# Optimization experiments

Hardware: AMD Instinct MI355X
Metric: run time of the kernel (lower is better)

The kernel has to match this reference:

```python
import jax, jax.numpy as jnp
import numpy as np

B, S, D, H = 64, 128, 1024, 8
DK = D // H  # 128 == S, required by the module's (attn@V)@V quirk
DFF = 2048
EPS = 1e-12


def layernorm(x, w, b):
    u = x.mean(-1, keepdims=True)
    s = ((x - u) ** 2).mean(-1, keepdims=True)
    return w * (x - u) / jnp.sqrt(s + EPS) + b


def setup_inputs() -> dict:
    key = jax.random.key(0)
    ks = jax.random.split(key, 10)
    w = lambda k, shape: jax.random.normal(k, shape, jnp.float32) * 0.02
    return {
        "x": jax.random.normal(ks[0], (B, S, D), jnp.float32),
        "mask": jnp.ones((1, 1, S, S), jnp.int32),
        "Wq": w(ks[1], (D, D)), "bq": jnp.zeros((D,), jnp.float32),
        "Wk": w(ks[2], (D, D)), "bk": jnp.zeros((D,), jnp.float32),
        "Wv": w(ks[3], (D, D)), "bv": jnp.zeros((D,), jnp.float32),
        "Wo": w(ks[4], (D, D)), "bo": jnp.zeros((D,), jnp.float32),
        "ln1_w": jnp.ones((D,), jnp.float32), "ln1_b": jnp.zeros((D,), jnp.float32),
        "W1": w(ks[5], (DFF, D)), "b1": jnp.zeros((DFF,), jnp.float32),
        "W2": w(ks[6], (4 * D, DFF)), "b2": jnp.zeros((4 * D,), jnp.float32),
        "W3": w(ks[7], (D, 4 * D)), "b3": jnp.zeros((D,), jnp.float32),
        "ln2_w": jnp.ones((D,), jnp.float32), "ln2_b": jnp.zeros((D,), jnp.float32),
    }


def reference(x, mask, Wq, bq, Wk, bk, Wv, bv, Wo, bo, ln1_w, ln1_b,
              W1, b1, W2, b2, W3, b3, ln2_w, ln2_b):
    # QKV projections -> [B, H, S, DK]
    Q = (x @ Wq.T + bq).reshape(B, S, H, DK).transpose(0, 2, 1, 3)
    K = (x @ Wk.T + bk).reshape(B, S, H, DK).transpose(0, 2, 1, 3)
    V = (x @ Wv.T + bv).reshape(B, S, H, DK).transpose(0, 2, 1, 3)

    scores = jnp.einsum('bhqd,bhkd->bhqk', Q, K) / jnp.sqrt(jnp.float32(DK))
    scores = jnp.where(mask == 0, jnp.float32(-1e9), scores)
    attn = jax.nn.softmax(scores, axis=-1)  # dropout = identity (eval)
    av = jnp.matmul(attn, V)                 # [B,H,S,DK]
    # Faithful quirk in the source: multiply by V a second time (DK == S).
    ctx = jnp.matmul(av, V)                  # [B,H,S,DK]
    ctx = ctx.transpose(0, 2, 1, 3).reshape(B, S, D)
    attn_out = ctx @ Wo.T + bo

    h = layernorm(x + attn_out, ln1_w, ln1_b)

    f = jax.nn.relu(h @ W1.T + b1)           # [B,S,DFF]
    f = jax.nn.relu(f @ W2.T + b2)           # [B,S,4D]
    f = f @ W3.T + b3                        # [B,S,D]

    return layernorm(h + f, ln2_w, ln2_b)
```

## Files before the change

kernel.cpp:

```cpp
#include <hip/hip_runtime.h>
#include <hip/hip_bf16.h>

using bf16 = __hip_bfloat16;
typedef __attribute__((ext_vector_type(4))) float f32x4;
typedef __attribute__((ext_vector_type(8))) short bf16x8;

__device__ __forceinline__ unsigned short bfbits(float f) {
    bf16 h = __float2bfloat16(f);
    return __builtin_bit_cast(unsigned short, h);
}

__device__ __forceinline__ void g2l16(const void* g, void* l) {
    __builtin_amdgcn_global_load_lds(
        (const __attribute__((address_space(1))) unsigned int*)g,
        (__attribute__((address_space(3))) unsigned int*)l, 16, 0, 0);
}

__global__ void castk(const float* __restrict__ in, bf16* __restrict__ out, int n4) {
    int stride = gridDim.x * blockDim.x;
    for (int i = blockIdx.x * blockDim.x + threadIdx.x; i < n4; i += stride) {
        float4 v = reinterpret_cast<const float4*>(in)[i];
        ushort4 o;
        o.x = bfbits(v.x); o.y = bfbits(v.y); o.z = bfbits(v.z); o.w = bfbits(v.w);
        reinterpret_cast<ushort4*>(out)[i] = o;
    }
}

template<int EPI>
__global__ __launch_bounds__(256, 2)
void gemm_bt(const bf16* __restrict__ A, const bf16* __restrict__ Bm,
             int M, int N, int K,
             const float* __restrict__ bias0, const float* __restrict__ bias1,
             const float* __restrict__ bias2, const float* __restrict__ resid,
             void* __restrict__ outp,
             bf16* __restrict__ q_o, bf16* __restrict__ k_o, bf16* __restrict__ v_o) {
    (void)M;
    __shared__ __align__(16) char As[8192];
    __shared__ __align__(16) char Bs[8192];
    int tid = threadIdx.x, wave = tid >> 6, lane = tid & 63;
    int nbn = N >> 7;
    int bm = blockIdx.x / nbn, bn = blockIdx.x % nbn;
    int wm = (wave >> 1) << 6, wn = (wave & 1) << 6;
    int rlo = lane & 15, g = lane >> 4;

    const char* abase = (const char*)(A + (size_t)(bm << 7) * K);
    const char* bbase = (const char*)(Bm + (size_t)(bn << 7) * K);

    const f32x4 fzero = {0.f, 0.f, 0.f, 0.f};
    f32x4 acc[4][4];
#pragma unroll
    for (int i = 0; i < 4; ++i)
#pragma unroll
        for (int j = 0; j < 4; ++j) acc[i][j] = fzero;

    int L0 = wave * 2048 + lane * 16;
    size_t ldbyte = (size_t)K * 2;

    for (int k0 = 0; k0 < K; k0 += 32) {
#pragma unroll
        for (int j = 0; j < 2; ++j) {
            int L = L0 + j * 1024;
            int row = L >> 6;
            int cb = (L & 63) ^ (((row >> 1) & 3) << 4);
            g2l16(abase + (size_t)row * ldbyte + (size_t)k0 * 2 + cb, As + wave * 2048 + j * 1024);
            g2l16(bbase + (size_t)row * ldbyte + (size_t)k0 * 2 + cb, Bs + wave * 2048 + j * 1024);
        }
        __syncthreads();
        bf16x8 af[4], bf8[4];
#pragma unroll
        for (int i = 0; i < 4; ++i) {
            int ra = wm + i * 16 + rlo;
            af[i] = *reinterpret_cast<const bf16x8*>(As + ra * 64 + ((g * 16) ^ (((ra >> 1) & 3) << 4)));
            int rb = wn + i * 16 + rlo;
            bf8[i] = *reinterpret_cast<const bf16x8*>(Bs + rb * 64 + ((g * 16) ^ (((rb >> 1) & 3) << 4)));
        }
#pragma unroll
        for (int mi = 0; mi < 4; ++mi)
#pragma unroll
            for (int ni = 0; ni < 4; ++ni)
                acc[mi][ni] = __builtin_amdgcn_mfma_f32_16x16x32_bf16(af[mi], bf8[ni], acc[mi][ni], 0, 0, 0);
        __syncthreads();
    }

    int gm0 = (bm << 7) + wm, gn0 = (bn << 7) + wn;
#pragma unroll
    for (int mi = 0; mi < 4; ++mi) {
#pragma unroll
        for (int ni = 0; ni < 4; ++ni) {
            int gnc = gn0 + ni * 16 + rlo;
#pragma unroll
            for (int r = 0; r < 4; ++r) {
                int gmr = gm0 + mi * 16 + g * 4 + r;
                float val = acc[mi][ni][r];
                if constexpr (EPI == 0) {
                    int t = gnc >> 10;
                    const float* bp = (t == 0) ? bias0 : ((t == 1) ? bias1 : bias2);
                    val += bp[gnc & 1023];
                    bf16* dst = (t == 0) ? q_o : ((t == 1) ? k_o : v_o);
                    int hh = (gnc >> 7) & 7, d = gnc & 127;
                    int bb = gmr >> 7, s = gmr & 127;
                    dst[(((size_t)bb * 8 + hh) * 128 + s) * 128 + d] = __float2bfloat16(val);
                } else if constexpr (EPI == 1) {
                    val = fmaxf(val + bias0[gnc], 0.f);
                    ((bf16*)outp)[(size_t)gmr * N + gnc] = __float2bfloat16(val);
                } else {
                    val += bias0[gnc] + resid[(size_t)gmr * N + gnc];
                    ((float*)outp)[(size_t)gmr * N + gnc] = val;
                }
            }
        }
    }
}

__global__ __launch_bounds__(256)
void transpose_v(const bf16* __restrict__ V, bf16* __restrict__ VT) {
    __shared__ unsigned short t[128 * 132];
    int bh = blockIdx.x, tid = threadIdx.x;
    const unsigned short* src = (const unsigned short*)(V + (size_t)bh * 16384);
#pragma unroll
    for (int i = 0; i < 8; ++i) {
        int idx = tid + i * 256;
        int srow = idx >> 4;
        int c8 = (idx & 15) * 8;
        ushort4 a = reinterpret_cast<const ushort4*>(src + srow * 128 + c8)[0];
        ushort4 b = reinterpret_cast<const ushort4*>(src + srow * 128 + c8 + 4)[0];
        reinterpret_cast<ushort4*>(t + srow * 132 + c8)[0] = a;
        reinterpret_cast<ushort4*>(t + srow * 132 + c8 + 4)[0] = b;
    }
    __syncthreads();
    unsigned short* dst = (unsigned short*)(VT + (size_t)bh * 16384);
#pragma unroll
    for (int i = 0; i < 8; ++i) {
        int idx = tid + i * 256;
        int drow = idx >> 4;
        int s8 = (idx & 15) * 8;
        ushort4 a, b;
        a.x = t[(s8 + 0) * 132 + drow]; a.y = t[(s8 + 1) * 132 + drow];
        a.z = t[(s8 + 2) * 132 + drow]; a.w = t[(s8 + 3) * 132 + drow];
        b.x = t[(s8 + 4) * 132 + drow]; b.y = t[(s8 + 5) * 132 + drow];
        b.z = t[(s8 + 6) * 132 + drow]; b.w = t[(s8 + 7) * 132 + drow];
        reinterpret_cast<ushort4*>(dst + drow * 128 + s8)[0] = a;
        reinterpret_cast<ushort4*>(dst + drow * 128 + s8 + 4)[0] = b;
    }
}

__global__ __launch_bounds__(256, 2)
void attn_scores(const bf16* __restrict__ Q, const bf16* __restrict__ K, bf16* __restrict__ P) {
    __shared__ __align__(16) char Qs[32768];
    __shared__ __align__(16) char Ks[32768];
    int bh = blockIdx.x;
    int tid = threadIdx.x, wave = tid >> 6, lane = tid & 63;
    const char* qsrc = (const char*)(Q + (size_t)bh * 16384);
    const char* ksrc = (const char*)(K + (size_t)bh * 16384);
#pragma unroll
    for (int j = 0; j < 8; ++j) {
        int L = wave * 8192 + j * 1024 + lane * 16;
        int row = L >> 8;
        int cb = (L & 255) ^ ((row & 7) << 4);
        g2l16(qsrc + row * 256 + cb, Qs + wave * 8192 + j * 1024);
        g2l16(ksrc + row * 256 + cb, Ks + wave * 8192 + j * 1024);
    }
    __syncthreads();
    int rlo = lane & 15, g = lane >> 4;
    const f32x4 fzero = {0.f, 0.f, 0.f, 0.f};
    f32x4 acc[2][8];
#pragma unroll
    for (int mi = 0; mi < 2; ++mi)
#pragma unroll
        for (int ni = 0; ni < 8; ++ni) acc[mi][ni] = fzero;
#pragma unroll
    for (int kk = 0; kk < 4; ++kk) {
        bf16x8 aq[2], bk8[8];
#pragma unroll
        for (int mi = 0; mi < 2; ++mi) {
            int row = wave * 32 + mi * 16 + rlo;
            aq[mi] = *reinterpret_cast<const bf16x8*>(Qs + row * 256 + ((kk * 64 + g * 16) ^ ((row & 7) << 4)));
        }
#pragma unroll
        for (int ni = 0; ni < 8; ++ni) {
            int row = ni * 16 + rlo;
            bk8[ni] = *reinterpret_cast<const bf16x8*>(Ks + row * 256 + ((kk * 64 + g * 16) ^ ((row & 7) << 4)));
        }
#pragma unroll
        for (int mi = 0; mi < 2; ++mi)
#pragma unroll
            for (int ni = 0; ni < 8; ++ni)
                acc[mi][ni] = __builtin_amdgcn_mfma_f32_16x16x32_bf16(aq[mi], bk8[ni], acc[mi][ni], 0, 0, 0);
    }
    const float scale = 0.088388347648318447f;
    unsigned short* pdst = (unsigned short*)(P + (size_t)bh * 16384);
#pragma unroll
    for (int mi = 0; mi < 2; ++mi) {
#pragma unroll
        for (int r = 0; r < 4; ++r) {
            float m = -3e38f;
#pragma unroll
            for (int ni = 0; ni < 8; ++ni) m = fmaxf(m, acc[mi][ni][r]);
#pragma unroll
            for (int o = 1; o < 16; o <<= 1) m = fmaxf(m, __shfl_xor(m, o));
            m *= scale;
            float e[8];
            float sum = 0.f;
#pragma unroll
            for (int ni = 0; ni < 8; ++ni) { e[ni] = __expf(acc[mi][ni][r] * scale - m); sum += e[ni]; }
#pragma unroll
            for (int o = 1; o < 16; o <<= 1) sum += __shfl_xor(sum, o);
            float inv = 1.f / sum;
            int qrow = wave * 32 + mi * 16 + g * 4 + r;
#pragma unroll
            for (int ni = 0; ni < 8; ++ni)
                pdst[qrow * 128 + ni * 16 + rlo] = bfbits(e[ni] * inv);
        }
    }
}

__global__ __launch_bounds__(256, 2)
void attn_ctx(const bf16* __restrict__ P, const bf16* __restrict__ VT, bf16* __restrict__ CTX) {
    __shared__ __align__(16) char Vs[32768];
    __shared__ __align__(16) char Ts[32768];
    int bh = blockIdx.x, b = bh >> 3, h = bh & 7;
    int tid = threadIdx.x, wave = tid >> 6, lane = tid & 63;
    const char* vsrc = (const char*)(VT + (size_t)bh * 16384);
#pragma unroll
    for (int j = 0; j < 8; ++j) {
        int L = wave * 8192 + j * 1024 + lane * 16;
        int row = L >> 8;
        int cb = (L & 255) ^ ((row & 7) << 4);
        g2l16(vsrc + row * 256 + cb, Vs + wave * 8192 + j * 1024);
    }
    __syncthreads();
    int rlo = lane & 15, g = lane >> 4;
    const char* psrc = (const char*)(P + (size_t)bh * 16384);
    const f32x4 fzero = {0.f, 0.f, 0.f, 0.f};
    f32x4 accT[2][8];
#pragma unroll
    for (int mi = 0; mi < 2; ++mi)
#pragma unroll
        for (int ni = 0; ni < 8; ++ni) accT[mi][ni] = fzero;
#pragma unroll
    for (int kk = 0; kk < 4; ++kk) {
        bf16x8 ap[2], bv8[8];
#pragma unroll
        for (int mi = 0; mi < 2; ++mi) {
            int row = wave * 32 + mi * 16 + rlo;
            ap[mi] = *reinterpret_cast<const bf16x8*>(psrc + (size_t)row * 256 + kk * 64 + g * 16);
        }
#pragma unroll
        for (int ni = 0; ni < 8; ++ni) {
            int row = ni * 16 + rlo;
            bv8[ni] = *reinterpret_cast<const bf16x8*>(Vs + row * 256 + ((kk * 64 + g * 16) ^ ((row & 7) << 4)));
        }
#pragma unroll
        for (int mi = 0; mi < 2; ++mi)
#pragma unroll
            for (int ni = 0; ni < 8; ++ni)
                accT[mi][ni] = __builtin_amdgcn_mfma_f32_16x16x32_bf16(ap[mi], bv8[ni], accT[mi][ni], 0, 0, 0);
    }
#pragma unroll
    for (int mi = 0; mi < 2; ++mi)
#pragma unroll
        for (int ni = 0; ni < 8; ++ni)
#pragma unroll
            for (int r = 0; r < 4; ++r) {
                int trow = wave * 32 + mi * 16 + g * 4 + r;
                int cbyte = ((ni * 16 + rlo) * 2) ^ ((trow & 7) << 4);
                *(unsigned short*)(Ts + trow * 256 + cbyte) = bfbits(accT[mi][ni][r]);
            }
    __syncthreads();
    f32x4 accC[2][8];
#pragma unroll
    for (int mi = 0; mi < 2; ++mi)
#pragma unroll
        for (int ni = 0; ni < 8; ++ni) accC[mi][ni] = fzero;
#pragma unroll
    for (int kk = 0; kk < 4; ++kk) {
        bf16x8 at[2], bv8[8];
#pragma unroll
        for (int mi = 0; mi < 2; ++mi) {
            int row = wave * 32 + mi * 16 + rlo;
            at[mi] = *reinterpret_cast<const bf16x8*>(Ts + row * 256 + ((kk * 64 + g * 16) ^ ((row & 7) << 4)));
        }
#pragma unroll
        for (int ni = 0; ni < 8; ++ni) {
            int row = ni * 16 + rlo;
            bv8[ni] = *reinterpret_cast<const bf16x8*>(Vs + row * 256 + ((kk * 64 + g * 16) ^ ((row & 7) << 4)));
        }
#pragma unroll
        for (int mi = 0; mi < 2; ++mi)
#pragma unroll
            for (int ni = 0; ni < 8; ++ni)
                accC[mi][ni] = __builtin_amdgcn_mfma_f32_16x16x32_bf16(at[mi], bv8[ni], accC[mi][ni], 0, 0, 0);
    }
    unsigned short* cdst = (unsigned short*)CTX;
#pragma unroll
    for (int mi = 0; mi < 2; ++mi)
#pragma unroll
        for (int ni = 0; ni < 8; ++ni)
#pragma unroll
            for (int r = 0; r < 4; ++r) {
                int q = wave * 32 + mi * 16 + g * 4 + r;
                int gm = b * 128 + q;
                int col = h * 128 + ni * 16 + rlo;
                cdst[(size_t)gm * 1024 + col] = bfbits(accC[mi][ni][r]);
            }
}

template<int MODE>
__global__ __launch_bounds__(256)
void ln_k(const float* __restrict__ Y, const float* __restrict__ w, const float* __restrict__ b,
          float* __restrict__ Hf, bf16* __restrict__ Hb) {
    int row = blockIdx.x, tid = threadIdx.x;
    float4 v = reinterpret_cast<const float4*>(Y + (size_t)row * 1024)[tid];
    float s = v.x + v.y + v.z + v.w;
    float q = v.x * v.x + v.y * v.y + v.z * v.z + v.w * v.w;
#pragma unroll
    for (int o = 1; o < 64; o <<= 1) { s += __shfl_xor(s, o); q += __shfl_xor(q, o); }
    __shared__ float ss[4], sq[4];
    if ((tid & 63) == 0) { ss[tid >> 6] = s; sq[tid >> 6] = q; }
    __syncthreads();
    s = ss[0] + ss[1] + ss[2] + ss[3];
    q = sq[0] + sq[1] + sq[2] + sq[3];
    float u = s * (1.f / 1024.f);
    float var = fmaxf(q * (1.f / 1024.f) - u * u, 0.f);
    float rstd = rsqrtf(var + 1e-12f);
    float4 wv = reinterpret_cast<const float4*>(w)[tid];
    float4 bv = reinterpret_cast<const float4*>(b)[tid];
    float o0 = wv.x * (v.x - u) * rstd + bv.x;
    float o1 = wv.y * (v.y - u) * rstd + bv.y;
    float o2 = wv.z * (v.z - u) * rstd + bv.z;
    float o3 = wv.w * (v.w - u) * rstd + bv.w;
    reinterpret_cast<float4*>(Hf + (size_t)row * 1024)[tid] = make_float4(o0, o1, o2, o3);
    if constexpr (MODE == 0) {
        ushort4 ob;
        ob.x = bfbits(o0); ob.y = bfbits(o1); ob.z = bfbits(o2); ob.w = bfbits(o3);
        reinterpret_cast<ushort4*>(Hb)[row * 256 + tid] = ob;
    }
}

extern "C" void kernel_launch(void* const* d_in, const int* in_sizes, int n_in,
                              void* d_out, int out_size, void* d_ws, size_t ws_size,
                              hipStream_t stream) {
    (void)in_sizes; (void)n_in; (void)out_size; (void)ws_size;
    const float* x    = (const float*)d_in[0];
    const float* Wq   = (const float*)d_in[2];
    const float* bq   = (const float*)d_in[3];
    const float* Wk   = (const float*)d_in[4];
    const float* bk   = (const float*)d_in[5];
    const float* Wv   = (const float*)d_in[6];
    const float* bv   = (const float*)d_in[7];
    const float* Wo   = (const float*)d_in[8];
    const float* bo   = (const float*)d_in[9];
    const float* ln1w = (const float*)d_in[10];
    const float* ln1b = (const float*)d_in[11];
    const float* W1   = (const float*)d_in[12];
    const float* b1   = (const float*)d_in[13];
    const float* W2   = (const float*)d_in[14];
    const float* b2   = (const float*)d_in[15];
    const float* W3   = (const float*)d_in[16];
    const float* b3   = (const float*)d_in[17];
    const float* ln2w = (const float*)d_in[18];
    const float* ln2b = (const float*)d_in[19];

    char* ws = (char*)d_ws;
    bf16*  XB    = (bf16*)(ws + 0);
    bf16*  WQKVB = (bf16*)(ws + 16777216);
    bf16*  WOB   = (bf16*)(ws + 23068672);
    bf16*  W1B   = (bf16*)(ws + 25165824);
    bf16*  W2B   = (bf16*)(ws + 29360128);
    bf16*  W3B   = (bf16*)(ws + 46137344);
    bf16*  Qb    = (bf16*)(ws + 54525952);
    bf16*  Kb    = (bf16*)(ws + 71303168);
    bf16*  Vb    = (bf16*)(ws + 88080384);
    bf16*  VTb   = (bf16*)(ws + 104857600);
    bf16*  Pb    = (bf16*)(ws + 121634816);
    bf16*  CTX   = (bf16*)(ws + 138412032);
    float* Y2    = (float*)(ws + 155189248);
    float* H32   = (float*)(ws + 188743680);
    bf16*  HB    = (bf16*)(ws + 222298112);
    bf16*  F1    = (bf16*)(ws + 155189248);
    bf16*  F2    = (bf16*)(ws + 54525952);
    float* Y5    = (float*)(ws + 121634816);

    auto cast = [&](const float* s, bf16* dd, int n4) {
        int nb = (n4 + 255) / 256; if (nb > 2048) nb = 2048;
        castk<<<nb, 256, 0, stream>>>(s, dd, n4);
    };
    cast(x,  XB,             2097152);
    cast(Wq, WQKVB,           262144);
    cast(Wk, WQKVB + 1048576, 262144);
    cast(Wv, WQKVB + 2097152, 262144);
    cast(Wo, WOB,             262144);
    cast(W1, W1B,             524288);
    cast(W2, W2B,            2097152);
    cast(W3, W3B,            1048576);

    gemm_bt<0><<<1536, 256, 0, stream>>>(XB, WQKVB, 8192, 3072, 1024,
                                         bq, bk, bv, nullptr, nullptr, Qb, Kb, Vb);
    transpose_v<<<512, 256, 0, stream>>>(Vb, VTb);
    attn_scores<<<512, 256, 0, stream>>>(Qb, Kb, Pb);
    attn_ctx<<<512, 256, 0, stream>>>(Pb, VTb, CTX);
    gemm_bt<2><<<512, 256, 0, stream>>>(CTX, WOB, 8192, 1024, 1024,
                                        bo, nullptr, nullptr, x, (void*)Y2,
                                        nullptr, nullptr, nullptr);
    ln_k<0><<<8192, 256, 0, stream>>>(Y2, ln1w, ln1b, H32, HB);
    gemm_bt<1><<<1024, 256, 0, stream>>>(HB, W1B, 8192, 2048, 1024,
                                         b1, nullptr, nullptr, nullptr, (void*)F1,
                                         nullptr, nullptr, nullptr);
    gemm_bt<1><<<2048, 256, 0, stream>>>(F1, W2B, 8192, 4096, 2048,
                                         b2, nullptr, nullptr, nullptr, (void*)F2,
                                         nullptr, nullptr, nullptr);
    gemm_bt<2><<<512, 256, 0, stream>>>(F2, W3B, 8192, 1024, 4096,
                                        b3, nullptr, nullptr, H32, (void*)Y5,
                                        nullptr, nullptr, nullptr);
    ln_k<1><<<8192, 256, 0, stream>>>(Y5, ln2w, ln2b, (float*)d_out, nullptr);
}
```

Baseline: 499.8 us.

## Add 256x256-tile triple-buffered GEMM for QKV and FFN up-projections

Adds a new 512-thread GEMM kernel with 256x256 output tiles. It uses triple-buffered direct global-to-LDS loads with an XOR swizzle, splits each k-step into two half-steps separated by barriers, raises wave priority around the MFMAs and remaps workgroup IDs across XCDs. The QKV, W1 and W2 GEMMs move to this kernel to get more data reuse per tile and to overlap loads with compute, while the old kernel now only serves the residual epilogue. The trade-offs are 96KB of LDS per block, fewer blocks (384/256/512) that may underfill the 256 CUs, and heavier register pressure from the 8x4 accumulator array.

```diff
diff --git a/kernel.cpp b/kernel.cpp
--- a/kernel.cpp
+++ b/kernel.cpp
@@ -27,13 +27,139 @@
 }
 
 template<int EPI>
+__global__ __launch_bounds__(512, 2)
+void gemm256(const bf16* __restrict__ A, const bf16* __restrict__ Bm,
+             int N, int K,
+             const float* __restrict__ bias0, const float* __restrict__ bias1,
+             const float* __restrict__ bias2,
+             void* __restrict__ outp,
+             bf16* __restrict__ q_o, bf16* __restrict__ k_o, bf16* __restrict__ v_o) {
+    __shared__ __align__(16) char lds[98304];
+    const int tid = threadIdx.x;
+    const int lane = tid & 63, wave = tid >> 6;
+    const int rlo = lane & 15, g = lane >> 4;
+    const int wr = wave >> 2, wc = wave & 3;
+    const int nbn = N >> 8;
+    const int nwg = gridDim.x;
+    int wg = (int)blockIdx.x;
+    wg = (wg & 7) * (nwg >> 3) + (wg >> 3);
+    const int bm = wg / nbn, bn = wg % nbn;
+    const size_t ldb = (size_t)K * 2;
+    const char* abase = (const char*)A + ((size_t)bm << 8) * ldb;
+    const char* bbase = (const char*)Bm + ((size_t)bn << 8) * ldb;
+
+    const int P = tid * 16;
+    const int R = P >> 7;
+    const int qs = (P & 127) ^ ((R & 7) << 4);
+    const size_t goff0 = (size_t)(R * 2 + (qs >> 6)) * ldb + (qs & 63);
+    const size_t ghalf = (size_t)128 * ldb;
+
+    const int o_in = (((rlo & 1) << 6) | (g << 4)) ^ (((rlo >> 1) & 7) << 4);
+    const int aoff = wr * 8192 + (rlo >> 1) * 128 + o_in;
+    const int boff = 16384 + (wc >> 1) * 8192 + (wc & 1) * 4096 + (rlo >> 1) * 128 + o_in;
+
+    const f32x4 fz = {0.f, 0.f, 0.f, 0.f};
+    f32x4 acc[8][4];
+#pragma unroll
+    for (int i = 0; i < 8; ++i)
+#pragma unroll
+        for (int j = 0; j < 4; ++j) acc[i][j] = fz;
+
+    auto stA = [&](int buf, int h, int kt) {
+        g2l16(abase + goff0 + (size_t)h * ghalf + (size_t)kt * 64,
+              lds + buf * 32768 + h * 8192 + P);
+    };
+    auto stB = [&](int buf, int h, int kt) {
+        g2l16(bbase + goff0 + (size_t)h * ghalf + (size_t)kt * 64,
+              lds + buf * 32768 + 16384 + h * 8192 + P);
+    };
+
+    stA(0, 0, 0); stA(0, 1, 0); stB(0, 0, 0); stB(0, 1, 0);
+    stA(1, 0, 1); stA(1, 1, 1); stB(1, 0, 1); stB(1, 1, 1);
+    asm volatile("s_waitcnt vmcnt(4)" ::: "memory");
+    __builtin_amdgcn_s_barrier();
+
+    const int NT = K >> 5;
+    for (int kt = 0; kt < NT; ++kt) {
+        const int buf = kt % 3;
+        const int nbuf = (kt + 2) % 3;
+        const char* lb = lds + buf * 32768;
+        const bool pre = (kt + 2) < NT;
+
+        bf16x8 bfr[4], afr[4];
+#pragma unroll
+        for (int nf = 0; nf < 4; ++nf)
+            bfr[nf] = *reinterpret_cast<const bf16x8*>(lb + nf * 1024 + boff);
+#pragma unroll
+        for (int i = 0; i < 4; ++i)
+            afr[i] = *reinterpret_cast<const bf16x8*>(lb + i * 1024 + aoff);
+        if (pre) { stA(nbuf, 0, kt + 2); stA(nbuf, 1, kt + 2); }
+        __builtin_amdgcn_s_barrier();
+        asm volatile("s_waitcnt lgkmcnt(0)");
+        __builtin_amdgcn_s_setprio(1);
+#pragma unroll
+        for (int i = 0; i < 4; ++i)
+#pragma unroll
+            for (int nf = 0; nf < 4; ++nf)
+                acc[i][nf] = __builtin_amdgcn_mfma_f32_16x16x32_bf16(afr[i], bfr[nf], acc[i][nf], 0, 0, 0);
+        __builtin_amdgcn_s_setprio(0);
+        __builtin_amdgcn_s_barrier();
+
+#pragma unroll
+        for (int i = 0; i < 4; ++i)
+            afr[i] = *reinterpret_cast<const bf16x8*>(lb + (4 + i) * 1024 + aoff);
+        if (pre) { stB(nbuf, 0, kt + 2); stB(nbuf, 1, kt + 2); }
+        if (pre) {
+            asm volatile("s_waitcnt vmcnt(4)" ::: "memory");
+        } else if (kt + 1 < NT) {
+            asm volatile("s_waitcnt vmcnt(0)" ::: "memory");
+        }
+        __builtin_amdgcn_s_barrier();
+        asm volatile("s_waitcnt lgkmcnt(0)");
+        __builtin_amdgcn_s_setprio(1);
+#pragma unroll
+        for (int i = 0; i < 4; ++i)
+#pragma unroll
+            for (int nf = 0; nf < 4; ++nf)
+                acc[4 + i][nf] = __builtin_amdgcn_mfma_f32_16x16x32_bf16(afr[i], bfr[nf], acc[4 + i][nf], 0, 0, 0);
+        __builtin_amdgcn_s_setprio(0);
+        __builtin_amdgcn_s_barrier();
+    }
+
+    const int gm0 = (bm << 8) + wr * 128;
+    const int gn0 = (bn << 8) + wc * 64;
+#pragma unroll
+    for (int mf = 0; mf < 8; ++mf) {
+#pragma unroll
+        for (int nf = 0; nf < 4; ++nf) {
+            const int gnc = gn0 + nf * 16 + rlo;
+#pragma unroll
+            for (int r = 0; r < 4; ++r) {
+                const int gmr = gm0 + mf * 16 + g * 4 + r;
+                float val = acc[mf][nf][r];
+                if constexpr (EPI == 0) {
+                    int t = gnc >> 10;
+                    const float* bp = (t == 0) ? bias0 : ((t == 1) ? bias1 : bias2);
+                    val += bp[gnc & 1023];
+                    bf16* dst = (t == 0) ? q_o : ((t == 1) ? k_o : v_o);
+                    int hh = (gnc >> 7) & 7, d = gnc & 127;
+                    int bb = gmr >> 7, s = gmr & 127;
+                    dst[(((size_t)bb * 8 + hh) * 128 + s) * 128 + d] = __float2bfloat16(val);
+                } else {
+                    val = fmaxf(val + bias0[gnc], 0.f);
+                    ((bf16*)outp)[(size_t)gmr * N + gnc] = __float2bfloat16(val);
+                }
+            }
+        }
+    }
+}
+
+template<int EPI>
 __global__ __launch_bounds__(256, 2)
 void gemm_bt(const bf16* __restrict__ A, const bf16* __restrict__ Bm,
              int M, int N, int K,
-             const float* __restrict__ bias0, const float* __restrict__ bias1,
-             const float* __restrict__ bias2, const float* __restrict__ resid,
-             void* __restrict__ outp,
-             bf16* __restrict__ q_o, bf16* __restrict__ k_o, bf16* __restrict__ v_o) {
+             const float* __restrict__ bias0, const float* __restrict__ resid,
+             void* __restrict__ outp) {
     (void)M;
     __shared__ __align__(16) char As[8192];
     __shared__ __align__(16) char Bs[8192];
@@ -92,21 +218,8 @@
             for (int r = 0; r < 4; ++r) {
                 int gmr = gm0 + mi * 16 + g * 4 + r;
                 float val = acc[mi][ni][r];
-                if constexpr (EPI == 0) {
-                    int t = gnc >> 10;
-                    const float* bp = (t == 0) ? bias0 : ((t == 1) ? bias1 : bias2);
-                    val += bp[gnc & 1023];
-                    bf16* dst = (t == 0) ? q_o : ((t == 1) ? k_o : v_o);
-                    int hh = (gnc >> 7) & 7, d = gnc & 127;
-                    int bb = gmr >> 7, s = gmr & 127;
-                    dst[(((size_t)bb * 8 + hh) * 128 + s) * 128 + d] = __float2bfloat16(val);
-                } else if constexpr (EPI == 1) {
-                    val = fmaxf(val + bias0[gnc], 0.f);
-                    ((bf16*)outp)[(size_t)gmr * N + gnc] = __float2bfloat16(val);
-                } else {
-                    val += bias0[gnc] + resid[(size_t)gmr * N + gnc];
-                    ((float*)outp)[(size_t)gmr * N + gnc] = val;
-                }
+                val += bias0[gnc] + resid[(size_t)gmr * N + gnc];
+                ((float*)outp)[(size_t)gmr * N + gnc] = val;
             }
         }
     }
@@ -394,23 +507,17 @@
     cast(W2, W2B,            2097152);
     cast(W3, W3B,            1048576);
 
-    gemm_bt<0><<<1536, 256, 0, stream>>>(XB, WQKVB, 8192, 3072, 1024,
-                                         bq, bk, bv, nullptr, nullptr, Qb, Kb, Vb);
+    gemm256<0><<<384, 512, 0, stream>>>(XB, WQKVB, 3072, 1024,
+                                        bq, bk, bv, nullptr, Qb, Kb, Vb);
     transpose_v<<<512, 256, 0, stream>>>(Vb, VTb);
     attn_scores<<<512, 256, 0, stream>>>(Qb, Kb, Pb);
     attn_ctx<<<512, 256, 0, stream>>>(Pb, VTb, CTX);
-    gemm_bt<2><<<512, 256, 0, stream>>>(CTX, WOB, 8192, 1024, 1024,
-                                        bo, nullptr, nullptr, x, (void*)Y2,
-                                        nullptr, nullptr, nullptr);
+    gemm_bt<2><<<512, 256, 0, stream>>>(CTX, WOB, 8192, 1024, 1024, bo, x, (void*)Y2);
     ln_k<0><<<8192, 256, 0, stream>>>(Y2, ln1w, ln1b, H32, HB);
-    gemm_bt<1><<<1024, 256, 0, stream>>>(HB, W1B, 8192, 2048, 1024,
-                                         b1, nullptr, nullptr, nullptr, (void*)F1,
-                                         nullptr, nullptr, nullptr);
-    gemm_bt<1><<<2048, 256, 0, stream>>>(F1, W2B, 8192, 4096, 2048,
-                                         b2, nullptr, nullptr, nullptr, (void*)F2,
-                                         nullptr, nullptr, nullptr);
-    gemm_bt<2><<<512, 256, 0, stream>>>(F2, W3B, 8192, 1024, 4096,
-                                        b3, nullptr, nullptr, H32, (void*)Y5,
-                                        nullptr, nullptr, nullptr);
+    gemm256<1><<<256, 512, 0, stream>>>(HB, W1B, 2048, 1024,
+                                        b1, nullptr, nullptr, (void*)F1, nullptr, nullptr, nullptr);
+    gemm256<1><<<512, 512, 0, stream>>>(F1, W2B, 4096, 2048,
+                                        b2, nullptr, nullptr, (void*)F2, nullptr, nullptr, nullptr);
+    gemm_bt<2><<<512, 256, 0, stream>>>(F2, W3B, 8192, 1024, 4096, b3, H32, (void*)Y5);
     ln_k<1><<<8192, 256, 0, stream>>>(Y5, ln2w, ln2b, (float*)d_out, nullptr);
 }
```

After: 475.3 us. -4.9%, faster.
